# Kernel tuning notes

Hardware: AMD Instinct MI355X
Metric: run time of the kernel (lower is better)

The kernel has to match this reference:

```python
import jax, jax.numpy as jnp
import numpy as np

LN_EPS = 1e-12


def setup_inputs() -> dict:
    key = jax.random.key(0)
    k1, k2, k3, k4 = jax.random.split(key, 4)
    B, H, L, D = 2, 12, 2048, 64
    q = jax.random.normal(k1, (B, H, L, D), dtype=jnp.float32)
    k = jax.random.normal(k2, (B, H, L, D), dtype=jnp.float32)
    v = jax.random.normal(k3, (B, H, L, D), dtype=jnp.float32)
    mask = jax.random.randint(k4, (1, 1, L, L), 0, 2).astype(jnp.int32)
    gamma = jnp.ones((D,), dtype=jnp.float32)
    beta = jnp.zeros((D,), dtype=jnp.float32)
    return {"q": q, "k": k, "v": v, "mask": mask, "gamma": gamma, "beta": beta}


def reference(q, k, v, mask, gamma, beta):
    # score = q @ k^T  -> [B, H, L, L]
    score = jnp.einsum("bhqd,bhkd->bhqk", q, k)
    # masked_fill(mask == 0, -10000)
    score = jnp.where(mask == 0, jnp.float32(-10000.0), score)
    # result = score @ v -> [B, H, L, D]  (no softmax)
    result = jnp.einsum("bhqk,bhkd->bhqd", score, v)
    # layer norm over the last dim (d_tensor)
    mean = jnp.mean(result, axis=-1, keepdims=True)
    var = jnp.var(result, axis=-1, keepdims=True)
    normed = (result - mean) / jnp.sqrt(var + LN_EPS)
    return normed * gamma + beta
```

## Files before the change

kernel.cpp:

```cpp
#include <hip/hip_runtime.h>

#define SEQ 2048
#define HD 64
#define NBH 24
#define ROWB 144

#define MB_OFF   0
#define MB_BYTES (32 * 32 * 512)
#define QB_OFF   (MB_OFF + MB_BYTES)
#define QK_BYTES (NBH * SEQ * HD * 2)
#define KB_OFF   (QB_OFF + QK_BYTES)
#define VT_OFF   (KB_OFF + QK_BYTES)
#define WS_NEED  ((size_t)(VT_OFF + QK_BYTES))

typedef __bf16 bfrag8 __attribute__((ext_vector_type(8)));
typedef __bf16 bf16x4 __attribute__((ext_vector_type(4)));
typedef float  floatx4 __attribute__((ext_vector_type(4)));

__device__ __forceinline__ floatx4 mfma_16x16x32(bfrag8 a, bfrag8 b, floatx4 c) {
    return __builtin_amdgcn_mfma_f32_16x16x32_bf16(a, b, c, 0, 0, 0);
}

__global__ __launch_bounds__(256)
void prep_kernel(const float* __restrict__ qp, const float* __restrict__ kp,
                 const float* __restrict__ vp, const int* __restrict__ maskp,
                 unsigned char* __restrict__ ws)
{
    __shared__ __attribute__((aligned(16))) unsigned char parena[64 * 68 * 4];
    const int t = threadIdx.x;
    const int b = blockIdx.x;

    if (b < 1536) {
        int gt  = b * 256 + t;
        int row = gt >> 3;
        int c   = gt & 7;
        const floatx4* qs = (const floatx4*)(qp + row * 64 + c * 8);
        const floatx4* ks = (const floatx4*)(kp + row * 64 + c * 8);
        floatx4 q0 = qs[0], q1 = qs[1];
        floatx4 k0 = ks[0], k1 = ks[1];
        bfrag8 qpk, kpk;
        #pragma unroll
        for (int i = 0; i < 4; ++i) {
            qpk[i] = (__bf16)q0[i]; qpk[4 + i] = (__bf16)q1[i];
            kpk[i] = (__bf16)k0[i]; kpk[4 + i] = (__bf16)k1[i];
        }
        *(bfrag8*)(ws + QB_OFF + row * 128 + c * 16) = qpk;
        *(bfrag8*)(ws + KB_OFF + row * 128 + c * 16) = kpk;
    } else if (b < 2304) {
        int bb = b - 1536, bh = bb >> 5, kt = bb & 31;
        float* lf = (float*)parena;
        const floatx4* vg = (const floatx4*)(vp + (bh * SEQ + kt * 64) * 64);
        #pragma unroll
        for (int it = 0; it < 4; ++it) {
            int f = t + it * 256;
            int r = f >> 4, c4 = f & 15;
            floatx4 val = vg[f];
            #pragma unroll
            for (int i = 0; i < 4; ++i) lf[r * 68 + c4 * 4 + i] = val[i];
        }
        __syncthreads();
        int d = t >> 2, kseg = t & 3;
        unsigned char* tb = ws + VT_OFF + (size_t)(bh * 32 + kt) * 8192 + d * 128;
        #pragma unroll
        for (int jj = 0; jj < 2; ++jj) {
            bfrag8 pk;
            #pragma unroll
            for (int e = 0; e < 8; ++e)
                pk[e] = (__bf16)lf[(kseg * 16 + jj * 8 + e) * 68 + d];
            *(bfrag8*)(tb + (kseg * 2 + jj) * 16) = pk;
        }
    } else {
        int cc = b - 2304, qtb = cc >> 5, kt = cc & 31;
        const int w = t >> 6, lane = t & 63;
        #pragma unroll
        for (int it = 0; it < 16; ++it) {
            int rr = it * 4 + w;
            unsigned long long bl = __ballot(maskp[(qtb * 64 + rr) * SEQ + kt * 64 + lane] != 0);
            if (lane == 0)
                *(unsigned long long*)(ws + MB_OFF + (size_t)((qtb * 32 + kt) * 64 + rr) * 8) = bl;
        }
    }
}

__global__ __launch_bounds__(256, 3)
void normattn_main(const unsigned char* __restrict__ ws,
                   const float* __restrict__ gammap, const float* __restrict__ betap,
                   float* __restrict__ outp)
{
    __shared__ __attribute__((aligned(16))) unsigned char sK[2][64 * ROWB];
    __shared__ __attribute__((aligned(16))) unsigned char sV[2][64 * ROWB];
    __shared__ __attribute__((aligned(16))) unsigned char sS[2][64 * 128];

    const int tid  = threadIdx.x;
    const int w    = tid >> 6;
    const int lane = tid & 63;
    const int quad = lane >> 4;
    const int l16  = lane & 15;
    const int qtb  = blockIdx.x;
    const int bh   = blockIdx.y;
    const int q0   = qtb * 64;
    const int swz  = l16 & 7;

    const unsigned char* gKb = ws + KB_OFF + (size_t)(bh * SEQ) * 128;
    const unsigned char* gVb = ws + VT_OFF + (size_t)(bh * 32) * 8192;
    const unsigned char* gMb = ws + MB_OFF + (size_t)(qtb * 32) * 512;

    bfrag8 qb[4][2];
    #pragma unroll
    for (int qt = 0; qt < 4; ++qt) {
        const unsigned char* gQ = ws + QB_OFF + (size_t)(bh * SEQ + q0 + qt * 16 + l16) * 128 + quad * 16;
        qb[qt][0] = *(const bfrag8*)gQ;
        qb[qt][1] = *(const bfrag8*)(gQ + 64);
    }

    floatx4 acc[4];
    #pragma unroll
    for (int i = 0; i < 4; ++i) acc[i] = (floatx4)0.0f;
    const int qrow_loc = w * 16 + quad * 4;

    const int sr0 = tid >> 3, sc0 = tid & 7;
    const int sr1 = (tid + 256) >> 3, sc1 = tid & 7;

    auto load_tile = [&](int kt, bfrag8 (&kr)[2], bfrag8 (&vr)[2]) {
        const unsigned char* gK = gKb + (size_t)kt * 8192;
        const unsigned char* gV = gVb + (size_t)kt * 8192;
        kr[0] = *(const bfrag8*)(gK + tid * 16);
        kr[1] = *(const bfrag8*)(gK + (tid + 256) * 16);
        vr[0] = *(const bfrag8*)(gV + tid * 16);
        vr[1] = *(const bfrag8*)(gV + (tid + 256) * 16);
    };
    auto write_tile = [&](int s, bfrag8 (&kr)[2], bfrag8 (&vr)[2]) {
        *(bfrag8*)(&sK[s][0] + sr0 * ROWB + sc0 * 16) = kr[0];
        *(bfrag8*)(&sK[s][0] + sr1 * ROWB + sc1 * 16) = kr[1];
        *(bfrag8*)(&sV[s][0] + sr0 * ROWB + sc0 * 16) = vr[0];
        *(bfrag8*)(&sV[s][0] + sr1 * ROWB + sc1 * 16) = vr[1];
    };

    auto qk_phase = [&](int tt, const unsigned char* cK, const unsigned long long (&mr)[4]) {
        bfrag8 ka0 = *(const bfrag8*)(cK + (w * 16 + l16) * ROWB + quad * 16);
        bfrag8 ka1 = *(const bfrag8*)(cK + (w * 16 + l16) * ROWB + 64 + quad * 16);
        #pragma unroll
        for (int qt = 0; qt < 4; ++qt) {
            floatx4 st = (floatx4)0.0f;
            st = mfma_16x16x32(ka0, qb[qt][0], st);
            st = mfma_16x16x32(ka1, qb[qt][1], st);
            unsigned long long m4 = mr[qt] >> (w * 16 + quad * 4);
            bf16x4 pk;
            #pragma unroll
            for (int r = 0; r < 4; ++r) {
                float v = ((m4 >> r) & 1ull) ? st[r] : -10000.0f;
                pk[r] = (__bf16)v;
            }
            *(bf16x4*)(&sS[tt][0] + (qt * 16 + l16) * 128 +
                       (((w * 2 + (quad >> 1)) ^ swz) * 16) + (quad & 1) * 8) = pk;
        }
    };
    auto pv_phase = [&](int tt, const unsigned char* cV) {
        #pragma unroll
        for (int kc2 = 0; kc2 < 2; ++kc2) {
            bfrag8 pa = *(const bfrag8*)(&sS[tt][0] + (w * 16 + l16) * 128 +
                                         (((kc2 * 4 + quad) ^ swz) * 16));
            #pragma unroll
            for (int nt = 0; nt < 4; ++nt) {
                bfrag8 vb = *(const bfrag8*)(cV + (nt * 16 + l16) * ROWB + kc2 * 64 + quad * 16);
                acc[nt] = mfma_16x16x32(pa, vb, acc[nt]);
            }
        }
    };

    {
        bfrag8 k0r[2], v0r[2], k1r[2], v1r[2];
        load_tile(0, k0r, v0r);
        load_tile(1, k1r, v1r);
        write_tile(0, k0r, v0r);
        write_tile(1, k1r, v1r);
    }
    asm volatile("s_waitcnt lgkmcnt(0)" ::: "memory");
    asm volatile("s_barrier" ::: "memory");

    for (int i = 0; i < 16; ++i) {
        const int t0 = 2 * i, t1 = 2 * i + 1;

        bfrag8 kA[2], vA[2];
        if (i < 15) load_tile(t0 + 2, kA, vA);

        unsigned long long mr0[4], mr1[4];
        #pragma unroll
        for (int qt = 0; qt < 4; ++qt) {
            mr0[qt] = *(const unsigned long long*)(gMb + (size_t)t0 * 512 + (qt * 16 + l16) * 8);
            mr1[qt] = *(const unsigned long long*)(gMb + (size_t)t1 * 512 + (qt * 16 + l16) * 8);
        }

        qk_phase(0, &sK[0][0], mr0);
        qk_phase(1, &sK[1][0], mr1);
        asm volatile("s_waitcnt lgkmcnt(0)" ::: "memory");
        asm volatile("s_barrier" ::: "memory");

        bfrag8 kB[2], vB[2];
        if (i < 15) load_tile(t0 + 3, kB, vB);

        pv_phase(0, &sV[0][0]);
        pv_phase(1, &sV[1][0]);
        asm volatile("s_waitcnt lgkmcnt(0)" ::: "memory");
        asm volatile("s_barrier" ::: "memory");

        if (i < 15) {
            write_tile(0, kA, vA);
            write_tile(1, kB, vB);
        }
        asm volatile("s_waitcnt lgkmcnt(0)" ::: "memory");
        asm volatile("s_barrier" ::: "memory");
    }

    float g[4], bt[4];
    #pragma unroll
    for (int nt = 0; nt < 4; ++nt) {
        g[nt]  = gammap[nt * 16 + l16];
        bt[nt] = betap[nt * 16 + l16];
    }
    #pragma unroll
    for (int r = 0; r < 4; ++r) {
        float s = 0.0f, s2 = 0.0f;
        #pragma unroll
        for (int nt = 0; nt < 4; ++nt) { float x = acc[nt][r]; s += x; s2 += x * x; }
        #pragma unroll
        for (int off = 1; off < 16; off <<= 1) {
            s  += __shfl_xor(s, off);
            s2 += __shfl_xor(s2, off);
        }
        float mean = s * (1.0f / 64.0f);
        float var  = s2 * (1.0f / 64.0f) - mean * mean;
        float rstd = rsqrtf(var + 1e-12f);
        float* orow = outp + (size_t)(bh * SEQ + q0 + qrow_loc + r) * 64;
        #pragma unroll
        for (int nt = 0; nt < 4; ++nt)
            orow[nt * 16 + l16] = (acc[nt][r] - mean) * rstd * g[nt] + bt[nt];
    }
}

#define KROW 72
#define SROW 40
__global__ __launch_bounds__(256, 4)
void normattn_fallback(const float* __restrict__ qp, const float* __restrict__ kp,
                       const float* __restrict__ vp, const int* __restrict__ maskp,
                       const float* __restrict__ gammap, const float* __restrict__ betap,
                       float* __restrict__ outp)
{
    __shared__ __attribute__((aligned(16))) __bf16 sQ[64 * KROW];
    __shared__ __attribute__((aligned(16))) __bf16 sK[64 * KROW];
    __shared__ __attribute__((aligned(16))) __bf16 sV[64 * KROW];
    __shared__ __attribute__((aligned(16))) __bf16 sS[4][16 * SROW];
    __shared__ __attribute__((aligned(8)))  unsigned int sMw[64][2];

    const int tid = threadIdx.x, wave = tid >> 6, lane = tid & 63;
    const int quad = lane >> 4, l16 = lane & 15;
    const int q0 = blockIdx.x * 64, bh = blockIdx.y;
    const int base = bh * SEQ * HD;
    {
        const floatx4* qg = (const floatx4*)(qp + base + q0 * HD);
        #pragma unroll
        for (int it = 0; it < 4; ++it) {
            int idx = tid + it * 256, r = idx >> 4, c = idx & 15;
            floatx4 val = qg[idx];
            bf16x4 pk = {(__bf16)val[0], (__bf16)val[1], (__bf16)val[2], (__bf16)val[3]};
            *(bf16x4*)&sQ[r * KROW + c * 4] = pk;
        }
    }
    __syncthreads();
    bfrag8 qa0 = *(const bfrag8*)&sQ[(wave * 16 + l16) * KROW + quad * 8];
    bfrag8 qa1 = *(const bfrag8*)&sQ[(wave * 16 + l16) * KROW + quad * 8 + 32];
    floatx4 acc[4];
    #pragma unroll
    for (int i = 0; i < 4; ++i) acc[i] = (floatx4)0.0f;
    const int qrow_loc = wave * 16 + quad * 4;
    const int qrb = q0 + qrow_loc;
    for (int kb = 0; kb < SEQ; kb += 64) {
        __syncthreads();
        {
            const floatx4* kg = (const floatx4*)(kp + base + kb * HD);
            #pragma unroll
            for (int it = 0; it < 4; ++it) {
                int idx = tid + it * 256, r = idx >> 4, c = idx & 15;
                floatx4 val = kg[idx];
                bf16x4 pk = {(__bf16)val[0], (__bf16)val[1], (__bf16)val[2], (__bf16)val[3]};
                *(bf16x4*)&sK[r * KROW + c * 4] = pk;
            }
        }
        {
            int d = tid & 63;
            #pragma unroll
            for (int it = 0; it < 4; ++it) {
                int k4 = (tid >> 6) + it * 4;
                bf16x4 pk;
                #pragma unroll
                for (int i = 0; i < 4; ++i) pk[i] = (__bf16)vp[base + (kb + k4 * 4 + i) * HD + d];
                *(bf16x4*)&sV[d * KROW + k4 * 4] = pk;
            }
        }
        #pragma unroll
        for (int it = 0; it < 16; ++it) {
            int rr = it * 4 + wave;
            unsigned long long bl = __ballot(maskp[(q0 + rr) * SEQ + kb + lane] != 0);
            if (lane == 0) { sMw[rr][0] = (unsigned)bl; sMw[rr][1] = (unsigned)(bl >> 32); }
        }
        __syncthreads();
        unsigned long long mrow[4];
        #pragma unroll
        for (int r = 0; r < 4; ++r) mrow[r] = *(const unsigned long long*)&sMw[qrow_loc + r][0];
        #pragma unroll
        for (int kc = 0; kc < 64; kc += 32) {
            floatx4 s0 = (floatx4)0.0f, s1 = (floatx4)0.0f;
            bfrag8 b00 = *(const bfrag8*)&sK[(kc + l16) * KROW + quad * 8];
            bfrag8 b01 = *(const bfrag8*)&sK[(kc + l16) * KROW + quad * 8 + 32];
            bfrag8 b10 = *(const bfrag8*)&sK[(kc + 16 + l16) * KROW + quad * 8];
            bfrag8 b11 = *(const bfrag8*)&sK[(kc + 16 + l16) * KROW + quad * 8 + 32];
            s0 = mfma_16x16x32(qa0, b00, s0);
            s0 = mfma_16x16x32(qa1, b01, s0);
            s1 = mfma_16x16x32(qa0, b10, s1);
            s1 = mfma_16x16x32(qa1, b11, s1);
            #pragma unroll
            for (int r = 0; r < 4; ++r) {
                float v0 = ((mrow[r] >> (kc + l16)) & 1ull) ? s0[r] : -10000.0f;
                float v1 = ((mrow[r] >> (kc + 16 + l16)) & 1ull) ? s1[r] : -10000.0f;
                sS[wave][(quad * 4 + r) * SROW + l16] = (__bf16)v0;
                sS[wave][(quad * 4 + r) * SROW + 16 + l16] = (__bf16)v1;
            }
            asm volatile("s_waitcnt lgkmcnt(0)" ::: "memory");
            bfrag8 pa = *(const bfrag8*)&sS[wave][l16 * SROW + quad * 8];
            #pragma unroll
            for (int nt = 0; nt < 4; ++nt) {
                bfrag8 vb = *(const bfrag8*)&sV[(nt * 16 + l16) * KROW + kc + quad * 8];
                acc[nt] = mfma_16x16x32(pa, vb, acc[nt]);
            }
        }
    }
    float g[4], bt[4];
    #pragma unroll
    for (int nt = 0; nt < 4; ++nt) { g[nt] = gammap[nt * 16 + l16]; bt[nt] = betap[nt * 16 + l16]; }
    #pragma unroll
    for (int r = 0; r < 4; ++r) {
        float s = 0.0f, s2 = 0.0f;
        #pragma unroll
        for (int nt = 0; nt < 4; ++nt) { float xx = acc[nt][r]; s += xx; s2 += xx * xx; }
        #pragma unroll
        for (int off = 1; off < 16; off <<= 1) { s += __shfl_xor(s, off); s2 += __shfl_xor(s2, off); }
        float mean = s * (1.0f / 64.0f);
        float var = s2 * (1.0f / 64.0f) - mean * mean;
        float rstd = rsqrtf(var + 1e-12f);
        float* orow = outp + base + (qrb + r) * HD;
        #pragma unroll
        for (int nt = 0; nt < 4; ++nt)
            orow[nt * 16 + l16] = (acc[nt][r] - mean) * rstd * g[nt] + bt[nt];
    }
}

extern "C" void kernel_launch(void* const* d_in, const int* in_sizes, int n_in,
                              void* d_out, int out_size, void* d_ws, size_t ws_size,
                              hipStream_t stream) {
    const float* q     = (const float*)d_in[0];
    const float* k     = (const float*)d_in[1];
    const float* v     = (const float*)d_in[2];
    const int*   mask  = (const int*)d_in[3];
    const float* gamma = (const float*)d_in[4];
    const float* beta  = (const float*)d_in[5];
    float* out = (float*)d_out;

    dim3 grid(32, NBH);
    if (ws_size >= WS_NEED) {
        unsigned char* ws = (unsigned char*)d_ws;
        prep_kernel<<<3328, 256, 0, stream>>>(q, k, v, mask, ws);
        normattn_main<<<grid, 256, 0, stream>>>(ws, gamma, beta, out);
    } else {
        normattn_fallback<<<grid, 256, 0, stream>>>(q, k, v, mask, gamma, beta, out);
    }
}
```

Baseline: 151.1 us.

## Switch main kernel to 32x32x16 MFMA with register-resident score transpose

Rewrites the main attention loop to use 32x32x16 bf16 MFMAs computing S^T tiles. The masked scores are converted to bf16 and rearranged in registers with v_permlane32_swap, so they feed the PV MFMA directly instead of going through a shared-memory score buffer. Each wave handles 32 query rows and half of each 64-key tile, and the two partial accumulators are reduced through LDS before layer norm. This removes the sS round trip and cuts the loop from three barriers per tile pair to one per tile. The cost is a cross-wave reduction at the end and fewer independent MFMA chains per wave.

```diff
diff --git a/kernel.cpp b/kernel.cpp
--- a/kernel.cpp
+++ b/kernel.cpp
@@ -16,9 +16,13 @@
 typedef __bf16 bfrag8 __attribute__((ext_vector_type(8)));
 typedef __bf16 bf16x4 __attribute__((ext_vector_type(4)));
 typedef float  floatx4 __attribute__((ext_vector_type(4)));
+typedef float  floatx16 __attribute__((ext_vector_type(16)));
 
 __device__ __forceinline__ floatx4 mfma_16x16x32(bfrag8 a, bfrag8 b, floatx4 c) {
     return __builtin_amdgcn_mfma_f32_16x16x32_bf16(a, b, c, 0, 0, 0);
+}
+__device__ __forceinline__ floatx16 mfma_32x32x16(bfrag8 a, bfrag8 b, floatx16 c) {
+    return __builtin_amdgcn_mfma_f32_32x32x16_bf16(a, b, c, 0, 0, 0);
 }
 
 __global__ __launch_bounds__(256)
@@ -89,34 +93,31 @@
 {
     __shared__ __attribute__((aligned(16))) unsigned char sK[2][64 * ROWB];
     __shared__ __attribute__((aligned(16))) unsigned char sV[2][64 * ROWB];
-    __shared__ __attribute__((aligned(16))) unsigned char sS[2][64 * 128];
 
     const int tid  = threadIdx.x;
     const int w    = tid >> 6;
     const int lane = tid & 63;
-    const int quad = lane >> 4;
-    const int l16  = lane & 15;
+    const int l32  = lane & 31;
+    const int hi   = lane >> 5;
+    const int qh   = w & 1;
+    const int kh   = w >> 1;
     const int qtb  = blockIdx.x;
     const int bh   = blockIdx.y;
     const int q0   = qtb * 64;
-    const int swz  = l16 & 7;
 
     const unsigned char* gKb = ws + KB_OFF + (size_t)(bh * SEQ) * 128;
     const unsigned char* gVb = ws + VT_OFF + (size_t)(bh * 32) * 8192;
     const unsigned char* gMb = ws + MB_OFF + (size_t)(qtb * 32) * 512;
 
-    bfrag8 qb[4][2];
+    bfrag8 qb[4];
     #pragma unroll
-    for (int qt = 0; qt < 4; ++qt) {
-        const unsigned char* gQ = ws + QB_OFF + (size_t)(bh * SEQ + q0 + qt * 16 + l16) * 128 + quad * 16;
-        qb[qt][0] = *(const bfrag8*)gQ;
-        qb[qt][1] = *(const bfrag8*)(gQ + 64);
-    }
-
-    floatx4 acc[4];
-    #pragma unroll
-    for (int i = 0; i < 4; ++i) acc[i] = (floatx4)0.0f;
-    const int qrow_loc = w * 16 + quad * 4;
+    for (int dstep = 0; dstep < 4; ++dstep)
+        qb[dstep] = *(const bfrag8*)(ws + QB_OFF +
+                        (size_t)(bh * SEQ + q0 + qh * 32 + l32) * 128 + dstep * 32 + hi * 16);
+
+    floatx16 acc[2];
+    acc[0] = (floatx16)0.0f;
+    acc[1] = (floatx16)0.0f;
 
     const int sr0 = tid >> 3, sc0 = tid & 7;
     const int sr1 = (tid + 256) >> 3, sc1 = tid & 7;
@@ -136,38 +137,6 @@
         *(bfrag8*)(&sV[s][0] + sr1 * ROWB + sc1 * 16) = vr[1];
     };
 
-    auto qk_phase = [&](int tt, const unsigned char* cK, const unsigned long long (&mr)[4]) {
-        bfrag8 ka0 = *(const bfrag8*)(cK + (w * 16 + l16) * ROWB + quad * 16);
-        bfrag8 ka1 = *(const bfrag8*)(cK + (w * 16 + l16) * ROWB + 64 + quad * 16);
-        #pragma unroll
-        for (int qt = 0; qt < 4; ++qt) {
-            floatx4 st = (floatx4)0.0f;
-            st = mfma_16x16x32(ka0, qb[qt][0], st);
-            st = mfma_16x16x32(ka1, qb[qt][1], st);
-            unsigned long long m4 = mr[qt] >> (w * 16 + quad * 4);
-            bf16x4 pk;
-            #pragma unroll
-            for (int r = 0; r < 4; ++r) {
-                float v = ((m4 >> r) & 1ull) ? st[r] : -10000.0f;
-                pk[r] = (__bf16)v;
-            }
-            *(bf16x4*)(&sS[tt][0] + (qt * 16 + l16) * 128 +
-                       (((w * 2 + (quad >> 1)) ^ swz) * 16) + (quad & 1) * 8) = pk;
-        }
-    };
-    auto pv_phase = [&](int tt, const unsigned char* cV) {
-        #pragma unroll
-        for (int kc2 = 0; kc2 < 2; ++kc2) {
-            bfrag8 pa = *(const bfrag8*)(&sS[tt][0] + (w * 16 + l16) * 128 +
-                                         (((kc2 * 4 + quad) ^ swz) * 16));
-            #pragma unroll
-            for (int nt = 0; nt < 4; ++nt) {
-                bfrag8 vb = *(const bfrag8*)(cV + (nt * 16 + l16) * ROWB + kc2 * 64 + quad * 16);
-                acc[nt] = mfma_16x16x32(pa, vb, acc[nt]);
-            }
-        }
-    };
-
     {
         bfrag8 k0r[2], v0r[2], k1r[2], v1r[2];
         load_tile(0, k0r, v0r);
@@ -178,63 +147,103 @@
     asm volatile("s_waitcnt lgkmcnt(0)" ::: "memory");
     asm volatile("s_barrier" ::: "memory");
 
-    for (int i = 0; i < 16; ++i) {
-        const int t0 = 2 * i, t1 = 2 * i + 1;
-
-        bfrag8 kA[2], vA[2];
-        if (i < 15) load_tile(t0 + 2, kA, vA);
-
-        unsigned long long mr0[4], mr1[4];
-        #pragma unroll
-        for (int qt = 0; qt < 4; ++qt) {
-            mr0[qt] = *(const unsigned long long*)(gMb + (size_t)t0 * 512 + (qt * 16 + l16) * 8);
-            mr1[qt] = *(const unsigned long long*)(gMb + (size_t)t1 * 512 + (qt * 16 + l16) * 8);
-        }
-
-        qk_phase(0, &sK[0][0], mr0);
-        qk_phase(1, &sK[1][0], mr1);
+    const unsigned char* kbase = &sK[0][0] + (kh * 32 + l32) * ROWB + hi * 16;
+    const unsigned char* vbase = &sV[0][0] + l32 * ROWB + kh * 64 + hi * 16;
+
+    for (int kt = 0; kt < 32; ++kt) {
+        const int slot = kt & 1;
+        bfrag8 kN[2], vN[2];
+        if (kt < 30) load_tile(kt + 2, kN, vN);
+
+        const unsigned long long mrow =
+            *(const unsigned long long*)(gMb + (size_t)kt * 512 + (qh * 32 + l32) * 8);
+
+        floatx16 st = (floatx16)0.0f;
+        const unsigned char* cK = kbase + slot * (64 * ROWB);
+        #pragma unroll
+        for (int dstep = 0; dstep < 4; ++dstep) {
+            bfrag8 ka = *(const bfrag8*)(cK + dstep * 32);
+            st = mfma_32x32x16(ka, qb[dstep], st);
+        }
+
+        const unsigned bits = (unsigned)(mrow >> (kh * 32 + 4 * hi));
+        unsigned u[8];
+        #pragma unroll
+        for (int j = 0; j < 8; ++j) {
+            const int kl0 = 2 * (j & 1) + 8 * (j >> 1);
+            float a = ((bits >> kl0) & 1u) ? st[2 * j] : -10000.0f;
+            float b = ((bits >> (kl0 + 1)) & 1u) ? st[2 * j + 1] : -10000.0f;
+            asm("v_cvt_pk_bf16_f32 %0, %1, %2" : "=v"(u[j]) : "v"(a), "v"(b));
+        }
+        asm("v_permlane32_swap_b32 %0, %1" : "+v"(u[0]), "+v"(u[2]));
+        asm("v_permlane32_swap_b32 %0, %1" : "+v"(u[1]), "+v"(u[3]));
+        asm("v_permlane32_swap_b32 %0, %1" : "+v"(u[4]), "+v"(u[6]));
+        asm("v_permlane32_swap_b32 %0, %1" : "+v"(u[5]), "+v"(u[7]));
+        union { unsigned int w4[4]; bfrag8 f; } c0, c1;
+        c0.w4[0] = u[0]; c0.w4[1] = u[1]; c0.w4[2] = u[2]; c0.w4[3] = u[3];
+        c1.w4[0] = u[4]; c1.w4[1] = u[5]; c1.w4[2] = u[6]; c1.w4[3] = u[7];
+
+        const unsigned char* cV = vbase + slot * (64 * ROWB);
+        #pragma unroll
+        for (int dh = 0; dh < 2; ++dh) {
+            bfrag8 va0 = *(const bfrag8*)(cV + dh * 32 * ROWB);
+            bfrag8 va1 = *(const bfrag8*)(cV + dh * 32 * ROWB + 32);
+            acc[dh] = mfma_32x32x16(va0, c0.f, acc[dh]);
+            acc[dh] = mfma_32x32x16(va1, c1.f, acc[dh]);
+        }
+
         asm volatile("s_waitcnt lgkmcnt(0)" ::: "memory");
         asm volatile("s_barrier" ::: "memory");
-
-        bfrag8 kB[2], vB[2];
-        if (i < 15) load_tile(t0 + 3, kB, vB);
-
-        pv_phase(0, &sV[0][0]);
-        pv_phase(1, &sV[1][0]);
-        asm volatile("s_waitcnt lgkmcnt(0)" ::: "memory");
-        asm volatile("s_barrier" ::: "memory");
-
-        if (i < 15) {
-            write_tile(0, kA, vA);
-            write_tile(1, kB, vB);
-        }
-        asm volatile("s_waitcnt lgkmcnt(0)" ::: "memory");
-        asm volatile("s_barrier" ::: "memory");
-    }
-
-    float g[4], bt[4];
-    #pragma unroll
-    for (int nt = 0; nt < 4; ++nt) {
-        g[nt]  = gammap[nt * 16 + l16];
-        bt[nt] = betap[nt * 16 + l16];
-    }
-    #pragma unroll
-    for (int r = 0; r < 4; ++r) {
+        if (kt < 30) write_tile(slot, kN, vN);
+    }
+
+    float* ex = (float*)&sK[0][0];
+    const int exb = (qh * 64 + lane) * 32;
+    if (kh == 1) {
+        #pragma unroll
+        for (int dh = 0; dh < 2; ++dh)
+            #pragma unroll
+            for (int jj = 0; jj < 4; ++jj) {
+                floatx4 t;
+                #pragma unroll
+                for (int e = 0; e < 4; ++e) t[e] = acc[dh][jj * 4 + e];
+                *(floatx4*)(ex + exb + (((dh * 4 + jj) ^ (lane & 7)) * 4)) = t;
+            }
+    }
+    __syncthreads();
+    if (kh == 0) {
+        #pragma unroll
+        for (int dh = 0; dh < 2; ++dh)
+            #pragma unroll
+            for (int jj = 0; jj < 4; ++jj) {
+                floatx4 t = *(const floatx4*)(ex + exb + (((dh * 4 + jj) ^ (lane & 7)) * 4));
+                #pragma unroll
+                for (int e = 0; e < 4; ++e) acc[dh][jj * 4 + e] += t[e];
+            }
         float s = 0.0f, s2 = 0.0f;
         #pragma unroll
-        for (int nt = 0; nt < 4; ++nt) { float x = acc[nt][r]; s += x; s2 += x * x; }
-        #pragma unroll
-        for (int off = 1; off < 16; off <<= 1) {
-            s  += __shfl_xor(s, off);
-            s2 += __shfl_xor(s2, off);
-        }
+        for (int dh = 0; dh < 2; ++dh)
+            #pragma unroll
+            for (int r = 0; r < 16; ++r) { float x = acc[dh][r]; s += x; s2 += x * x; }
+        s  += __shfl_xor(s, 32);
+        s2 += __shfl_xor(s2, 32);
         float mean = s * (1.0f / 64.0f);
         float var  = s2 * (1.0f / 64.0f) - mean * mean;
         float rstd = rsqrtf(var + 1e-12f);
-        float* orow = outp + (size_t)(bh * SEQ + q0 + qrow_loc + r) * 64;
-        #pragma unroll
-        for (int nt = 0; nt < 4; ++nt)
-            orow[nt * 16 + l16] = (acc[nt][r] - mean) * rstd * g[nt] + bt[nt];
+        float* orow = outp + (size_t)(bh * SEQ + q0 + qh * 32 + l32) * 64;
+        #pragma unroll
+        for (int dh = 0; dh < 2; ++dh)
+            #pragma unroll
+            for (int jj = 0; jj < 4; ++jj) {
+                const int d0 = dh * 32 + jj * 8 + 4 * hi;
+                floatx4 gg = *(const floatx4*)(gammap + d0);
+                floatx4 bb = *(const floatx4*)(betap + d0);
+                floatx4 o;
+                #pragma unroll
+                for (int e = 0; e < 4; ++e)
+                    o[e] = (acc[dh][jj * 4 + e] - mean) * rstd * gg[e] + bb[e];
+                *(floatx4*)(orow + d0) = o;
+            }
     }
 }
 
```

Result: faster. 141.7 us (-6.2%).
